# Kernel tuning notes

Measured on AMD Instinct MI355X. Metric: run time of the kernel, lower is better.

Reference implementation:

```python
import jax, jax.numpy as jnp
import numpy as np

ALPHA = 0.0005
TAU = 0.2


def setup_inputs() -> dict:
    key = jax.random.key(0)
    k1, k2, k3 = jax.random.split(key, 3)
    output = jax.random.normal(k1, (8192, 1000), dtype=jnp.float32)
    target = jax.random.normal(k2, (8192, 1000), dtype=jnp.float32)
    conv_w = jax.random.normal(k3, (256, 256, 128, 3), dtype=jnp.float32)
    return {"output": output, "target": target, "conv_w": conv_w}


def reference(output, target, conv_w):
    # base loss (nn.MSELoss with default 'mean' reduction)
    loss = jnp.mean((output - target) ** 2)

    # Diversity regularizer: pairwise cosine similarity between slices
    # conv_w[:, :, i, :] along dim 2 ('filters' = size(2) in the original).
    F = conv_w.shape[2]
    # V: [F, D] with D = out_ch * in_ch * kw
    V = jnp.transpose(conv_w, (2, 0, 1, 3)).reshape(F, -1)
    norms = jnp.linalg.norm(V, axis=1)                      # [F]
    G = (V @ V.T) / (norms[:, None] * norms[None, :])       # [F, F] cosine Gram

    # keep entries with tau < sim <= 1 and i != j
    offdiag = ~jnp.eye(F, dtype=bool)
    mask = (G > TAU) & (G <= 1.0) & offdiag
    reg = jnp.sum(jnp.where(mask, G, jnp.zeros((), dtype=G.dtype)))

    return loss + ALPHA * reg
```

## Files before the change

### kernel.cpp

```cpp
#include <hip/hip_runtime.h>
#include <hip/hip_bf16.h>


typedef __attribute__((ext_vector_type(8))) short bf16x8;
typedef __attribute__((ext_vector_type(4))) float f32x4;

#define ALPHA 0.0005f
#define TAU 0.2f

#define FDIM 128
#define NPAIR 16
#define CHUNK_FLOATS 12288
#define DSTRIDE_DW 52
#define GRAM_NBLK 256
#define CHUNKS_PER_BLK 8
#define GRAM_ELEMS (FDIM * FDIM)
#define MSE_N4 2048000

#define AS1 __attribute__((address_space(1)))
#define AS3 __attribute__((address_space(3)))

__device__ inline void gl_lds16(const float* g, float* l) {
    __builtin_amdgcn_global_load_lds((AS1 const void*)g, (AS3 void*)l, 16, 0, 0);
}

__device__ inline unsigned int pack_bf2(float lo, float hi) {
    union { float f; unsigned int u; } a, b;
    a.f = lo; b.f = hi;
    unsigned int al = (a.u + 0x7fffu + ((a.u >> 16) & 1u)) >> 16;
    unsigned int bh = (b.u + 0x7fffu + ((b.u >> 16) & 1u)) & 0xffff0000u;
    return (al & 0xffffu) | bh;
}

__global__ void __launch_bounds__(256) fused_kernel(
        const float* __restrict__ o, const float* __restrict__ t,
        const float* __restrict__ conv,
        float* __restrict__ mse_part, float* __restrict__ partials) {
    __shared__ float raw[2][CHUNK_FLOATS];
    __shared__ unsigned int tile[FDIM * DSTRIDE_DW];
    __shared__ float red[4];
    const int tid = threadIdx.x;
    const int lane = tid & 63;
    const int wave = tid >> 6;
    const size_t blk_chunk0 = (size_t)blockIdx.x * CHUNKS_PER_BLK;

    {
        const float* g0 = conv + blk_chunk0 * CHUNK_FLOATS;
#pragma unroll
        for (int it = 0; it < 12; ++it)
            gl_lds16(g0 + (it * 256 + tid) * 4,
                     &raw[0][(it * 256 + wave * 64) * 4]);
    }

    {
        const int gid = blockIdx.x * 256 + tid;
        const float4* o4 = reinterpret_cast<const float4*>(o);
        const float4* t4 = reinterpret_cast<const float4*>(t);
        float s = 0.f;
        int i = gid;
#pragma unroll 4
        for (int k = 0; k < 31; ++k) {
            float4 a = o4[i], b = t4[i];
            float dx = a.x - b.x, dy = a.y - b.y, dz = a.z - b.z, dw = a.w - b.w;
            s += dx * dx + dy * dy + dz * dz + dw * dw;
            i += 65536;
        }
        if (gid < MSE_N4 - 31 * 65536) {
            float4 a = o4[i], b = t4[i];
            float dx = a.x - b.x, dy = a.y - b.y, dz = a.z - b.z, dw = a.w - b.w;
            s += dx * dx + dy * dy + dz * dz + dw * dw;
        }
        for (int off = 32; off; off >>= 1) s += __shfl_down(s, off);
        if (lane == 0) red[wave] = s;
        __syncthreads();
        if (tid == 0) mse_part[blockIdx.x] = red[0] + red[1] + red[2] + red[3];
    }

    f32x4 acc0[8], acc1[8];
#pragma unroll
    for (int cc = 0; cc < 8; ++cc) { acc0[cc] = (f32x4)0.f; acc1[cc] = (f32x4)0.f; }

    const int p = tid >> 4;
    const int q = tid & 15;
    const int colr = lane & 15;
    const int hi8 = (lane >> 4) * 8;
    const unsigned short* tileu = reinterpret_cast<const unsigned short*>(tile);

    for (int c = 0; c < CHUNKS_PER_BLK; ++c) {
        const int cur = c & 1;
        if (c + 1 < CHUNKS_PER_BLK) {
            const float* gn = conv + (blk_chunk0 + c + 1) * CHUNK_FLOATS;
            float* rn_ = &raw[cur ^ 1][0];
#pragma unroll
            for (int it = 0; it < 12; ++it)
                gl_lds16(gn + (it * 256 + tid) * 4, rn_ + (it * 256 + wave * 64) * 4);
            asm volatile("s_waitcnt vmcnt(12)" ::: "memory");
        } else {
            asm volatile("s_waitcnt vmcnt(0)" ::: "memory");
        }
        asm volatile("s_waitcnt lgkmcnt(0)" ::: "memory");
        __builtin_amdgcn_s_barrier();
        asm volatile("" ::: "memory");

        const float4* r0 = reinterpret_cast<const float4*>(&raw[cur][0])
                           + (2 * p) * 96 + q;
        const float4* r1 = r0 + 96;
#pragma unroll
        for (int it = 0; it < 6; ++it) {
            float4 v0 = r0[it * 16];
            float4 v1 = r1[it * 16];
            const int off4 = q + it * 16;
#pragma unroll
            for (int u = 0; u < 4; ++u) {
                const int idx = off4 * 4 + u;
                const int f = idx / 3;
                const int k = idx - f * 3;
                const float x0 = (u == 0) ? v0.x : (u == 1) ? v0.y : (u == 2) ? v0.z : v0.w;
                const float x1 = (u == 0) ? v1.x : (u == 1) ? v1.y : (u == 2) ? v1.z : v1.w;
                tile[f * DSTRIDE_DW + k * NPAIR + p] = pack_bf2(x0, x1);
            }
        }
        asm volatile("s_waitcnt lgkmcnt(0)" ::: "memory");
        __builtin_amdgcn_s_barrier();
        asm volatile("" ::: "memory");

#pragma unroll
        for (int ks = 0; ks < 3; ++ks) {
            const int koff = ks * 32 + hi8;
            bf16x8 a0 = *reinterpret_cast<const bf16x8*>(
                &tileu[(wave * 32 + colr) * (DSTRIDE_DW * 2) + koff]);
            bf16x8 a1 = *reinterpret_cast<const bf16x8*>(
                &tileu[(wave * 32 + 16 + colr) * (DSTRIDE_DW * 2) + koff]);
#pragma unroll
            for (int cc = 0; cc < 8; ++cc) {
                bf16x8 b = *reinterpret_cast<const bf16x8*>(
                    &tileu[(cc * 16 + colr) * (DSTRIDE_DW * 2) + koff]);
                acc0[cc] = __builtin_amdgcn_mfma_f32_16x16x32_bf16(a0, b, acc0[cc], 0, 0, 0);
                acc1[cc] = __builtin_amdgcn_mfma_f32_16x16x32_bf16(a1, b, acc1[cc], 0, 0, 0);
            }
        }
    }

    float* myp = partials + (size_t)blockIdx.x * GRAM_ELEMS;
    const int rsub = (lane >> 4) << 2;
#pragma unroll
    for (int cc = 0; cc < 8; ++cc) {
        const int col = cc * 16 + colr;
#pragma unroll
        for (int j = 0; j < 4; ++j) {
            const int r0w = wave * 32 + rsub + j;
            myp[r0w * FDIM + col] = acc0[cc][j];
            myp[(r0w + 16) * FDIM + col] = acc1[cc][j];
        }
    }
}

__global__ void __launch_bounds__(256) reduce_kernel(
        const float* __restrict__ partials, float* __restrict__ gram) {
    __shared__ float acc_s[64][5];
    const int tid = threadIdx.x;
    const int el = tid & 63;
    const int sl = tid >> 6;
    const int e = blockIdx.x * 64 + el;
    float s = 0.f;
#pragma unroll 8
    for (int b = sl * 64; b < sl * 64 + 64; ++b)
        s += partials[(size_t)b * GRAM_ELEMS + e];
    acc_s[el][sl] = s;
    __syncthreads();
    if (tid < 64)
        gram[blockIdx.x * 64 + tid] =
            acc_s[tid][0] + acc_s[tid][1] + acc_s[tid][2] + acc_s[tid][3];
}

__global__ void __launch_bounds__(256) finalize_kernel(
        const float* __restrict__ gram, const float* __restrict__ mse_part,
        float* __restrict__ out) {
    __shared__ float rn[FDIM];
    __shared__ float red[4];
    __shared__ float redm[4];
    const int tid = threadIdx.x;
    if (tid < FDIM) rn[tid] = rsqrtf(gram[tid * (FDIM + 1)]);
    __syncthreads();
    float s = 0.f;
    for (int i = tid; i < GRAM_ELEMS; i += 256) {
        const int row = i >> 7, col = i & 127;
        const float g = gram[i] * rn[row] * rn[col];
        if (row != col && g > TAU && g <= 1.0f) s += g;
    }
    float m = mse_part[tid];
    for (int off = 32; off; off >>= 1) {
        s += __shfl_down(s, off);
        m += __shfl_down(m, off);
    }
    if ((tid & 63) == 0) { red[tid >> 6] = s; redm[tid >> 6] = m; }
    __syncthreads();
    if (tid == 0)
        out[0] = (redm[0] + redm[1] + redm[2] + redm[3]) * (1.0f / 8192000.0f) +
                 ALPHA * (red[0] + red[1] + red[2] + red[3]);
}

extern "C" void kernel_launch(void* const* d_in, const int* in_sizes, int n_in,
                              void* d_out, int out_size, void* d_ws, size_t ws_size,
                              hipStream_t stream) {
    const float* output = (const float*)d_in[0];
    const float* target = (const float*)d_in[1];
    const float* conv   = (const float*)d_in[2];
    float* out = (float*)d_out;

    float* wsf      = (float*)d_ws;
    float* mse_part = wsf;
    float* gram     = wsf + 256;
    float* partials = wsf + 256 + GRAM_ELEMS;
    (void)ws_size;

    fused_kernel<<<GRAM_NBLK, 256, 0, stream>>>(output, target, conv,
                                                mse_part, partials);
    reduce_kernel<<<GRAM_ELEMS / 64, 256, 0, stream>>>(partials, gram);
    finalize_kernel<<<1, 256, 0, stream>>>(gram, mse_part, out);
}
```

Before: 62.81 us.

## Split MSE into its own kernel and register-prefetch Gram chunks across more blocks

Splits the fused kernel into a separate MSE reduction kernel and a Gram kernel. The Gram kernel now runs 512 blocks of 4 chunks each, loading chunks through registers with software double buffering instead of global-to-LDS async loads, and allows 2 blocks per CU. The reduce kernel now sums 512 partials. If the workspace is too small, a fallback path accumulates into the Gram matrix with atomics. This aims to raise occupancy and overlap loads with bf16 conversion and MFMA, at the cost of an extra launch and a larger partials buffer to reduce.

```diff
diff --git a/kernel.cpp b/kernel.cpp
--- a/kernel.cpp
+++ b/kernel.cpp
@@ -9,22 +9,14 @@
 #define TAU 0.2f
 
 #define FDIM 128
-#define NPAIR 16
-#define CHUNK_FLOATS 12288
-#define DSTRIDE_DW 52
-#define GRAM_NBLK 256
-#define CHUNKS_PER_BLK 8
+#define TSTRIDE_DW 52
+#define GRAM_NBLK 512
+#define CHUNK_F4 3072
 #define GRAM_ELEMS (FDIM * FDIM)
 #define MSE_N4 2048000
-
-#define AS1 __attribute__((address_space(1)))
-#define AS3 __attribute__((address_space(3)))
-
-__device__ inline void gl_lds16(const float* g, float* l) {
-    __builtin_amdgcn_global_load_lds((AS1 const void*)g, (AS3 void*)l, 16, 0, 0);
-}
-
-__device__ inline unsigned int pack_bf2(float lo, float hi) {
+#define MSE_NBLK 2048
+
+__device__ __forceinline__ unsigned int pack_bf2(float lo, float hi) {
     union { float f; unsigned int u; } a, b;
     a.f = lo; b.f = hi;
     unsigned int al = (a.u + 0x7fffu + ((a.u >> 16) & 1u)) >> 16;
@@ -32,125 +24,130 @@
     return (al & 0xffffu) | bh;
 }
 
-__global__ void __launch_bounds__(256) fused_kernel(
+__global__ void __launch_bounds__(256) mse_kernel(
         const float* __restrict__ o, const float* __restrict__ t,
-        const float* __restrict__ conv,
-        float* __restrict__ mse_part, float* __restrict__ partials) {
-    __shared__ float raw[2][CHUNK_FLOATS];
-    __shared__ unsigned int tile[FDIM * DSTRIDE_DW];
+        float* __restrict__ mse_part) {
     __shared__ float red[4];
+    const int tid = threadIdx.x;
+    const float4* o4 = reinterpret_cast<const float4*>(o);
+    const float4* t4 = reinterpret_cast<const float4*>(t);
+    float s = 0.f;
+    for (int i = blockIdx.x * 256 + tid; i < MSE_N4; i += MSE_NBLK * 256) {
+        float4 a = o4[i], b = t4[i];
+        float dx = a.x - b.x, dy = a.y - b.y, dz = a.z - b.z, dw = a.w - b.w;
+        s += dx * dx + dy * dy + dz * dz + dw * dw;
+    }
+    for (int off = 32; off; off >>= 1) s += __shfl_down(s, off);
+    if ((tid & 63) == 0) red[tid >> 6] = s;
+    __syncthreads();
+    if (tid == 0) mse_part[blockIdx.x] = red[0] + red[1] + red[2] + red[3];
+}
+
+__device__ __forceinline__ void loadc(const f32x4* __restrict__ src4,
+                                      size_t base4, f32x4 (&R)[12]) {
+#pragma unroll
+    for (int it = 0; it < 6; ++it) {
+        R[2 * it]     = src4[base4 + 16 * it];
+        R[2 * it + 1] = src4[base4 + 96 + 16 * it];
+    }
+}
+
+__device__ __forceinline__ void convertc(const f32x4 (&R)[12],
+                                         unsigned int* __restrict__ tb,
+                                         int p, int q) {
+#pragma unroll
+    for (int it = 0; it < 6; ++it)
+#pragma unroll
+        for (int u = 0; u < 4; ++u) {
+            const int idx = (q + 16 * it) * 4 + u;
+            const int f = idx / 3;
+            const int k = idx - 3 * f;
+            tb[f * TSTRIDE_DW + k * 16 + p] = pack_bf2(R[2 * it][u], R[2 * it + 1][u]);
+        }
+}
+
+__device__ __forceinline__ void barrier_tile() {
+    asm volatile("s_waitcnt lgkmcnt(0)" ::: "memory");
+    __builtin_amdgcn_sched_barrier(0);
+    __builtin_amdgcn_s_barrier();
+    __builtin_amdgcn_sched_barrier(0);
+}
+
+__device__ __forceinline__ void mfmaph(const unsigned short* __restrict__ tu,
+                                       int wave, int colr, int hi8,
+                                       f32x4 (&acc0)[8], f32x4 (&acc1)[8]) {
+#pragma unroll
+    for (int ks = 0; ks < 3; ++ks) {
+        const int koff = ks * 32 + hi8;
+        bf16x8 a0 = *reinterpret_cast<const bf16x8*>(
+            &tu[(wave * 32 + colr) * (TSTRIDE_DW * 2) + koff]);
+        bf16x8 a1 = *reinterpret_cast<const bf16x8*>(
+            &tu[(wave * 32 + 16 + colr) * (TSTRIDE_DW * 2) + koff]);
+#pragma unroll
+        for (int cc = 0; cc < 8; ++cc) {
+            bf16x8 b = *reinterpret_cast<const bf16x8*>(
+                &tu[(cc * 16 + colr) * (TSTRIDE_DW * 2) + koff]);
+            acc0[cc] = __builtin_amdgcn_mfma_f32_16x16x32_bf16(a0, b, acc0[cc], 0, 0, 0);
+            acc1[cc] = __builtin_amdgcn_mfma_f32_16x16x32_bf16(a1, b, acc1[cc], 0, 0, 0);
+        }
+    }
+}
+
+template <int ATOMIC>
+__global__ void __launch_bounds__(256, 2) gram_kernel(
+        const float* __restrict__ conv, float* __restrict__ out) {
+    __shared__ unsigned int tile[2][FDIM * TSTRIDE_DW];
     const int tid = threadIdx.x;
     const int lane = tid & 63;
     const int wave = tid >> 6;
-    const size_t blk_chunk0 = (size_t)blockIdx.x * CHUNKS_PER_BLK;
-
-    {
-        const float* g0 = conv + blk_chunk0 * CHUNK_FLOATS;
-#pragma unroll
-        for (int it = 0; it < 12; ++it)
-            gl_lds16(g0 + (it * 256 + tid) * 4,
-                     &raw[0][(it * 256 + wave * 64) * 4]);
-    }
-
-    {
-        const int gid = blockIdx.x * 256 + tid;
-        const float4* o4 = reinterpret_cast<const float4*>(o);
-        const float4* t4 = reinterpret_cast<const float4*>(t);
-        float s = 0.f;
-        int i = gid;
-#pragma unroll 4
-        for (int k = 0; k < 31; ++k) {
-            float4 a = o4[i], b = t4[i];
-            float dx = a.x - b.x, dy = a.y - b.y, dz = a.z - b.z, dw = a.w - b.w;
-            s += dx * dx + dy * dy + dz * dz + dw * dw;
-            i += 65536;
-        }
-        if (gid < MSE_N4 - 31 * 65536) {
-            float4 a = o4[i], b = t4[i];
-            float dx = a.x - b.x, dy = a.y - b.y, dz = a.z - b.z, dw = a.w - b.w;
-            s += dx * dx + dy * dy + dz * dz + dw * dw;
-        }
-        for (int off = 32; off; off >>= 1) s += __shfl_down(s, off);
-        if (lane == 0) red[wave] = s;
-        __syncthreads();
-        if (tid == 0) mse_part[blockIdx.x] = red[0] + red[1] + red[2] + red[3];
-    }
-
-    f32x4 acc0[8], acc1[8];
-#pragma unroll
-    for (int cc = 0; cc < 8; ++cc) { acc0[cc] = (f32x4)0.f; acc1[cc] = (f32x4)0.f; }
-
     const int p = tid >> 4;
     const int q = tid & 15;
     const int colr = lane & 15;
     const int hi8 = (lane >> 4) * 8;
-    const unsigned short* tileu = reinterpret_cast<const unsigned short*>(tile);
-
-    for (int c = 0; c < CHUNKS_PER_BLK; ++c) {
-        const int cur = c & 1;
-        if (c + 1 < CHUNKS_PER_BLK) {
-            const float* gn = conv + (blk_chunk0 + c + 1) * CHUNK_FLOATS;
-            float* rn_ = &raw[cur ^ 1][0];
-#pragma unroll
-            for (int it = 0; it < 12; ++it)
-                gl_lds16(gn + (it * 256 + tid) * 4, rn_ + (it * 256 + wave * 64) * 4);
-            asm volatile("s_waitcnt vmcnt(12)" ::: "memory");
-        } else {
-            asm volatile("s_waitcnt vmcnt(0)" ::: "memory");
-        }
-        asm volatile("s_waitcnt lgkmcnt(0)" ::: "memory");
-        __builtin_amdgcn_s_barrier();
-        asm volatile("" ::: "memory");
-
-        const float4* r0 = reinterpret_cast<const float4*>(&raw[cur][0])
-                           + (2 * p) * 96 + q;
-        const float4* r1 = r0 + 96;
-#pragma unroll
-        for (int it = 0; it < 6; ++it) {
-            float4 v0 = r0[it * 16];
-            float4 v1 = r1[it * 16];
-            const int off4 = q + it * 16;
-#pragma unroll
-            for (int u = 0; u < 4; ++u) {
-                const int idx = off4 * 4 + u;
-                const int f = idx / 3;
-                const int k = idx - f * 3;
-                const float x0 = (u == 0) ? v0.x : (u == 1) ? v0.y : (u == 2) ? v0.z : v0.w;
-                const float x1 = (u == 0) ? v1.x : (u == 1) ? v1.y : (u == 2) ? v1.z : v1.w;
-                tile[f * DSTRIDE_DW + k * NPAIR + p] = pack_bf2(x0, x1);
-            }
-        }
-        asm volatile("s_waitcnt lgkmcnt(0)" ::: "memory");
-        __builtin_amdgcn_s_barrier();
-        asm volatile("" ::: "memory");
-
-#pragma unroll
-        for (int ks = 0; ks < 3; ++ks) {
-            const int koff = ks * 32 + hi8;
-            bf16x8 a0 = *reinterpret_cast<const bf16x8*>(
-                &tileu[(wave * 32 + colr) * (DSTRIDE_DW * 2) + koff]);
-            bf16x8 a1 = *reinterpret_cast<const bf16x8*>(
-                &tileu[(wave * 32 + 16 + colr) * (DSTRIDE_DW * 2) + koff]);
-#pragma unroll
-            for (int cc = 0; cc < 8; ++cc) {
-                bf16x8 b = *reinterpret_cast<const bf16x8*>(
-                    &tileu[(cc * 16 + colr) * (DSTRIDE_DW * 2) + koff]);
-                acc0[cc] = __builtin_amdgcn_mfma_f32_16x16x32_bf16(a0, b, acc0[cc], 0, 0, 0);
-                acc1[cc] = __builtin_amdgcn_mfma_f32_16x16x32_bf16(a1, b, acc1[cc], 0, 0, 0);
-            }
-        }
-    }
-
-    float* myp = partials + (size_t)blockIdx.x * GRAM_ELEMS;
+    const unsigned short* t0u = reinterpret_cast<const unsigned short*>(tile[0]);
+    const unsigned short* t1u = reinterpret_cast<const unsigned short*>(tile[1]);
+
+    f32x4 acc0[8], acc1[8];
+#pragma unroll
+    for (int cc = 0; cc < 8; ++cc) { acc0[cc] = (f32x4)0.f; acc1[cc] = (f32x4)0.f; }
+
+    const f32x4* src4 = reinterpret_cast<const f32x4*>(conv);
+    const size_t cb = (size_t)blockIdx.x * (4 * CHUNK_F4) + (2 * p) * 96 + q;
+
+    f32x4 RA[12], RB[12];
+    loadc(src4, cb + 0 * CHUNK_F4, RA);
+
+    loadc(src4, cb + 1 * CHUNK_F4, RB);
+    convertc(RA, tile[0], p, q);
+    barrier_tile();
+    mfmaph(t0u, wave, colr, hi8, acc0, acc1);
+    loadc(src4, cb + 2 * CHUNK_F4, RA);
+    convertc(RB, tile[1], p, q);
+    barrier_tile();
+    mfmaph(t1u, wave, colr, hi8, acc0, acc1);
+    loadc(src4, cb + 3 * CHUNK_F4, RB);
+    convertc(RA, tile[0], p, q);
+    barrier_tile();
+    mfmaph(t0u, wave, colr, hi8, acc0, acc1);
+    convertc(RB, tile[1], p, q);
+    barrier_tile();
+    mfmaph(t1u, wave, colr, hi8, acc0, acc1);
+
+    float* my = ATOMIC ? out : out + (size_t)blockIdx.x * GRAM_ELEMS;
     const int rsub = (lane >> 4) << 2;
 #pragma unroll
     for (int cc = 0; cc < 8; ++cc) {
         const int col = cc * 16 + colr;
 #pragma unroll
         for (int j = 0; j < 4; ++j) {
-            const int r0w = wave * 32 + rsub + j;
-            myp[r0w * FDIM + col] = acc0[cc][j];
-            myp[(r0w + 16) * FDIM + col] = acc1[cc][j];
+            const int r0 = wave * 32 + rsub + j;
+            if (ATOMIC) {
+                atomicAdd(&my[r0 * FDIM + col], acc0[cc][j]);
+                atomicAdd(&my[(r0 + 16) * FDIM + col], acc1[cc][j]);
+            } else {
+                my[r0 * FDIM + col] = acc0[cc][j];
+                my[(r0 + 16) * FDIM + col] = acc1[cc][j];
+            }
         }
     }
 }
@@ -163,8 +160,8 @@
     const int sl = tid >> 6;
     const int e = blockIdx.x * 64 + el;
     float s = 0.f;
-#pragma unroll 8
-    for (int b = sl * 64; b < sl * 64 + 64; ++b)
+#pragma unroll 16
+    for (int b = sl * 128; b < sl * 128 + 128; ++b)
         s += partials[(size_t)b * GRAM_ELEMS + e];
     acc_s[el][sl] = s;
     __syncthreads();
@@ -188,7 +185,9 @@
         const float g = gram[i] * rn[row] * rn[col];
         if (row != col && g > TAU && g <= 1.0f) s += g;
     }
-    float m = mse_part[tid];
+    float m = 0.f;
+#pragma unroll 8
+    for (int j = 0; j < 8; ++j) m += mse_part[tid * 8 + j];
     for (int off = 32; off; off >>= 1) {
         s += __shfl_down(s, off);
         m += __shfl_down(m, off);
@@ -210,12 +209,20 @@
 
     float* wsf      = (float*)d_ws;
     float* mse_part = wsf;
-    float* gram     = wsf + 256;
-    float* partials = wsf + 256 + GRAM_ELEMS;
-    (void)ws_size;
-
-    fused_kernel<<<GRAM_NBLK, 256, 0, stream>>>(output, target, conv,
-                                                mse_part, partials);
-    reduce_kernel<<<GRAM_ELEMS / 64, 256, 0, stream>>>(partials, gram);
+    float* gram     = wsf + MSE_NBLK;
+    float* partials = wsf + MSE_NBLK + GRAM_ELEMS;
+
+    const size_t need =
+        (MSE_NBLK + GRAM_ELEMS + (size_t)GRAM_NBLK * GRAM_ELEMS) * sizeof(float);
+
+    if (ws_size >= need) {
+        gram_kernel<0><<<GRAM_NBLK, 256, 0, stream>>>(conv, partials);
+        mse_kernel<<<MSE_NBLK, 256, 0, stream>>>(output, target, mse_part);
+        reduce_kernel<<<GRAM_ELEMS / 64, 256, 0, stream>>>(partials, gram);
+    } else {
+        hipMemsetAsync(gram, 0, GRAM_ELEMS * sizeof(float), stream);
+        gram_kernel<1><<<GRAM_NBLK, 256, 0, stream>>>(conv, gram);
+        mse_kernel<<<MSE_NBLK, 256, 0, stream>>>(output, target, mse_part);
+    }
     finalize_kernel<<<1, 256, 0, stream>>>(gram, mse_part, out);
 }
```

Result: no change. 62.03 us (-1.2%).
